# Optimization experiments

Measured on AMD Instinct MI355X. Metric: run time of the kernel, lower is better.

## Reference

```python
import jax, jax.numpy as jnp
import numpy as np

B = 8          # batch
RES = 64       # resolution (H = W)
DIM = 512      # channels
HEADS = 8
HD = DIM // HEADS   # 64
HSP, WSP = RES, 8   # idx=0: H_sp=resolution, W_sp=split_size
NH, NW = RES // HSP, RES // WSP   # windows per axis


def setup_inputs() -> dict:
    key = jax.random.key(0)
    k1, k2, k3 = jax.random.split(key, 3)
    qkv = jax.random.normal(k1, (3, B, RES * RES, DIM), dtype=jnp.float32)
    lepe_w = jax.random.normal(k2, (DIM, 1, 3, 3), dtype=jnp.float32) * 0.1
    lepe_b = jax.random.normal(k3, (DIM,), dtype=jnp.float32) * 0.1
    return {"qkv": qkv, "lepe_w": lepe_w, "lepe_b": lepe_b}


def _to_windows(t):
    # [B, L, C] row-major -> [B*NH*NW, HSP*WSP, C]; equivalent to the
    # block-diagonal flex_attention mask grouping (y//H_sp, x//W_sp).
    t = t.reshape(B, NH, HSP, NW, WSP, DIM)
    return t.transpose(0, 1, 3, 2, 4, 5).reshape(B * NH * NW, HSP * WSP, DIM)


def _from_windows(t):
    t = t.reshape(B, NH, NW, HSP, WSP, DIM).transpose(0, 1, 3, 2, 4, 5)
    return t.reshape(B, RES * RES, DIM)


def reference(qkv, lepe_w, lepe_b):
    q, k, v = qkv[0], qkv[1], qkv[2]            # each [B, L, C]
    qw, kw, vw = _to_windows(q), _to_windows(k), _to_windows(v)

    # LePE: depthwise 3x3 conv on v laid out per-window as [n, C, HSP, WSP]
    vimg = vw.transpose(0, 2, 1).reshape(-1, DIM, HSP, WSP)
    lepe = jax.lax.conv_general_dilated(
        vimg, lepe_w, window_strides=(1, 1), padding='SAME',
        dimension_numbers=('NCHW', 'OIHW', 'NCHW'), feature_group_count=DIM)
    lepe = lepe + lepe_b[None, :, None, None]
    lepe = lepe.reshape(-1, DIM, HSP * WSP).transpose(0, 2, 1)  # [n, T, C]

    def split_heads(t):
        return t.reshape(t.shape[0], t.shape[1], HEADS, HD)

    qh, kh, vh, lh = map(split_heads, (qw, kw, vw, lepe))
    scale = 1.0 / np.sqrt(HD).astype(np.float32)  # flex_attention default scale
    scores = jnp.einsum('wqhd,wkhd->whqk', qh, kh) * scale
    attn = jax.nn.softmax(scores, axis=-1)
    out = jnp.einsum('whqk,wkhd->wqhd', attn, vh) + lh   # [n, T, H, hd]
    out = out.reshape(out.shape[0], out.shape[1], DIM)
    return _from_windows(out)
```

## Files before the change

kernel.cpp:

```cpp
#include <hip/hip_runtime.h>
#include <hip/hip_bf16.h>

#define DIMV 512
#define HDV  64
#define VSTR 524
#define VT_BASE 65536
#define SMEM_B (VT_BASE + 64 * VSTR * 2)

typedef __bf16 bf16x8_t __attribute__((ext_vector_type(8)));
typedef float f32x4_t __attribute__((ext_vector_type(4)));

union Frag { bf16x8_t v; unsigned short u[8]; unsigned int w[4]; uint2 d[2]; uint4 q; };

static __device__ __forceinline__ unsigned short f2bf(float f) {
  return __builtin_bit_cast(unsigned short, (__bf16)f);
}
static __device__ __forceinline__ float bf2f(unsigned int h) {
  return __builtin_bit_cast(float, h << 16);
}
static __device__ __forceinline__ uint2 pack4(const float4 f) {
  uint2 r;
  r.x = (unsigned)f2bf(f.x) | ((unsigned)f2bf(f.y) << 16);
  r.y = (unsigned)f2bf(f.z) | ((unsigned)f2bf(f.w) << 16);
  return r;
}

#define BARRIER_NODRAIN() asm volatile("s_waitcnt lgkmcnt(0)\n\ts_barrier" ::: "memory")

__global__ __launch_bounds__(1024, 4)
void lepe_attn_kernel(const float* __restrict__ qkv,
                      const float* __restrict__ lw,
                      const float* __restrict__ lb,
                      float* __restrict__ out)
{
  __shared__ __align__(16) unsigned char smem[SMEM_B];

  const int wb   = blockIdx.x;
  const int win  = wb >> 2;
  const int bat  = win >> 3;
  const int nw   = win & 7;
  const int headbase = (wb & 3) << 1;

  const int tid  = threadIdx.x;
  const int wave = tid >> 6, lane = tid & 63;
  const int l15  = lane & 15, g = lane >> 4;

  const float* qptr = qkv;
  const float* kptr = qkv + 16777216;
  const float* vptr = qkv + 33554432;
  const int rowbase = bat * 4096;

  auto grow = [&](int tok) -> int {
    return rowbase + ((tok >> 3) << 6) + (nw << 3) + (tok & 7);
  };

  const int s_t = tid >> 4;
  const int s_c = (tid & 15) * 4;
  const size_t TSTRIDE = 262144;
  const size_t base_st = (size_t)grow(s_t) * DIMV + s_c;

  const int lr    = s_t & 31;
  const int tb0   = (s_t >> 5) * 4096;
  const int kfrag = (lr >> 4) * 2048 + (s_c >> 5) * 1024
                  + ((lr & 15) + 16 * ((s_c >> 3) & 3)) * 16 + (s_c & 7) * 2;

  unsigned short* vt = (unsigned short*)(smem + VT_BASE);

  float4 ck0, ck1, cv0, cv1;
  float4 qin[8];

  auto issueC = [&](int head, int c) {
    const float* kgp = kptr + base_st + head * HDV;
    const float* vgp = vptr + base_st + head * HDV;
    ck0 = *(const float4*)(kgp + (size_t)(2 * c) * TSTRIDE);
    ck1 = *(const float4*)(kgp + (size_t)(2 * c + 1) * TSTRIDE);
    cv0 = *(const float4*)(vgp + (size_t)(2 * c) * TSTRIDE);
    cv1 = *(const float4*)(vgp + (size_t)(2 * c + 1) * TSTRIDE);
  };
  auto writeC = [&](int c) {
    *(uint2*)(smem + c * 16384 + tb0 + kfrag)        = pack4(ck0);
    *(uint2*)(smem + c * 16384 + 8192 + tb0 + kfrag) = pack4(ck1);
    int t0 = s_t + 128 * c;
    vt[(s_c + 0) * VSTR + t0] = f2bf(cv0.x);
    vt[(s_c + 1) * VSTR + t0] = f2bf(cv0.y);
    vt[(s_c + 2) * VSTR + t0] = f2bf(cv0.z);
    vt[(s_c + 3) * VSTR + t0] = f2bf(cv0.w);
    int t1 = t0 + 64;
    vt[(s_c + 0) * VSTR + t1] = f2bf(cv1.x);
    vt[(s_c + 1) * VSTR + t1] = f2bf(cv1.y);
    vt[(s_c + 2) * VSTR + t1] = f2bf(cv1.z);
    vt[(s_c + 3) * VSTR + t1] = f2bf(cv1.w);
  };

  const float QSC = 0.1803368801f;
  const int qbase = wave * 32;
  size_t qoff[2];
  qoff[0] = (size_t)grow(qbase + l15) * DIMV;
  qoff[1] = (size_t)grow(qbase + 16 + l15) * DIMV;

  Frag qf[2][2];
  auto issueQ = [&](int head) {
    #pragma unroll
    for (int qi = 0; qi < 2; ++qi) {
      const float* qp = qptr + qoff[qi] + head * HDV;
      #pragma unroll
      for (int kc = 0; kc < 2; ++kc) {
        qin[qi * 4 + kc * 2 + 0] = *(const float4*)(qp + kc * 32 + 8 * g);
        qin[qi * 4 + kc * 2 + 1] = *(const float4*)(qp + kc * 32 + 8 * g + 4);
      }
    }
  };
  auto buildQF = [&]() {
    #pragma unroll
    for (int qi = 0; qi < 2; ++qi)
      #pragma unroll
      for (int kc = 0; kc < 2; ++kc) {
        const float4 f0 = qin[qi * 4 + kc * 2 + 0];
        const float4 f1 = qin[qi * 4 + kc * 2 + 1];
        qf[qi][kc].u[0] = f2bf(f0.x * QSC); qf[qi][kc].u[1] = f2bf(f0.y * QSC);
        qf[qi][kc].u[2] = f2bf(f0.z * QSC); qf[qi][kc].u[3] = f2bf(f0.w * QSC);
        qf[qi][kc].u[4] = f2bf(f1.x * QSC); qf[qi][kc].u[5] = f2bf(f1.y * QSC);
        qf[qi][kc].u[6] = f2bf(f1.z * QSC); qf[qi][kc].u[7] = f2bf(f1.w * QSC);
      }
  };

  issueC(headbase, 0);
  issueQ(headbase);
  writeC(0);
  buildQF();
  __syncthreads();

  const f32x4_t zero4 = {0.f, 0.f, 0.f, 0.f};
  const unsigned char* kfb = smem + lane * 16;

  #pragma unroll
  for (int p = 0; p < 2; ++p) {
    const int head = headbase + p;

    f32x4_t ot[4][2];
    #pragma unroll
    for (int di = 0; di < 4; ++di)
      #pragma unroll
      for (int qi = 0; qi < 2; ++qi) ot[di][qi] = zero4;
    float lsum[2] = {0.f, 0.f};

    #pragma unroll
    for (int c = 0; c < 4; ++c) {
      if (c < 3) issueC(head, c + 1);

      #pragma unroll
      for (int t4 = 0; t4 < 4; ++t4) {
        const int kt = c * 4 + t4;

        Frag kf[2][2];
        #pragma unroll
        for (int ki = 0; ki < 2; ++ki)
          #pragma unroll
          for (int kc = 0; kc < 2; ++kc)
            kf[ki][kc].q = *(const uint4*)(kfb + kt * 4096 + ki * 2048 + kc * 1024);

        f32x4_t st[2][2];
        #pragma unroll
        for (int ki = 0; ki < 2; ++ki)
          #pragma unroll
          for (int qi = 0; qi < 2; ++qi) st[ki][qi] = zero4;

        __builtin_amdgcn_s_setprio(1);
        #pragma unroll
        for (int kc = 0; kc < 2; ++kc)
          #pragma unroll
          for (int ki = 0; ki < 2; ++ki)
            #pragma unroll
            for (int qi = 0; qi < 2; ++qi)
              st[ki][qi] = __builtin_amdgcn_mfma_f32_16x16x32_bf16(
                  kf[ki][kc].v, qf[qi][kc].v, st[ki][qi], 0, 0, 0);
        __builtin_amdgcn_s_setprio(0);

        #pragma unroll
        for (int ki = 0; ki < 2; ++ki)
          #pragma unroll
          for (int qi = 0; qi < 2; ++qi) {
            f32x4_t s = st[ki][qi];
            #pragma unroll
            for (int r = 0; r < 4; ++r) {
              float pr = __builtin_amdgcn_exp2f(s[r]);
              s[r] = pr;
              lsum[qi] += pr;
            }
            st[ki][qi] = s;
          }

        Frag vf[4];
        #pragma unroll
        for (int di = 0; di < 4; ++di) {
          const unsigned char* vp = smem + VT_BASE + (di * 16 + l15) * (VSTR * 2)
                                    + kt * 64 + 8 * g;
          vf[di].d[0] = *(const uint2*)(vp);
          vf[di].d[1] = *(const uint2*)(vp + 32);
        }

        __builtin_amdgcn_s_setprio(1);
        #pragma unroll
        for (int qi = 0; qi < 2; ++qi) {
          Frag pb;
          #pragma unroll
          for (int r = 0; r < 4; ++r) {
            pb.u[r]     = f2bf(st[0][qi][r]);
            pb.u[4 + r] = f2bf(st[1][qi][r]);
          }
          #pragma unroll
          for (int di = 0; di < 4; ++di)
            ot[di][qi] = __builtin_amdgcn_mfma_f32_16x16x32_bf16(
                vf[di].v, pb.v, ot[di][qi], 0, 0, 0);
        }
        __builtin_amdgcn_s_setprio(0);
      }

      if (c < 3) { writeC(c + 1); BARRIER_NODRAIN(); }
    }

    float rl[2];
    #pragma unroll
    for (int qi = 0; qi < 2; ++qi) {
      float s = lsum[qi];
      s += __shfl_xor(s, 16, 64);
      s += __shfl_xor(s, 32, 64);
      rl[qi] = 1.0f / s;
    }

    float lout[32];
    {
      float wgt[9];
      const float* wp = lw + (size_t)(head * HDV + lane) * 9;
      #pragma unroll
      for (int i = 0; i < 9; ++i) wgt[i] = wp[i];
      const float bias = lb[head * HDV + lane];
      const int yb = wave * 4;

      float rm[8], rc[8], rp2[8];
      auto loadrow = [&](int y, float* dst) {
        if ((unsigned)y < 64u) {
          const unsigned char* pp = smem + VT_BASE + lane * (VSTR * 2) + y * 16;
          unsigned a0 = *(const unsigned*)(pp);
          unsigned a1 = *(const unsigned*)(pp + 4);
          unsigned a2 = *(const unsigned*)(pp + 8);
          unsigned a3 = *(const unsigned*)(pp + 12);
          dst[0] = bf2f(a0 & 0xffffu); dst[1] = bf2f(a0 >> 16);
          dst[2] = bf2f(a1 & 0xffffu); dst[3] = bf2f(a1 >> 16);
          dst[4] = bf2f(a2 & 0xffffu); dst[5] = bf2f(a2 >> 16);
          dst[6] = bf2f(a3 & 0xffffu); dst[7] = bf2f(a3 >> 16);
        } else {
          #pragma unroll
          for (int x = 0; x < 8; ++x) dst[x] = 0.f;
        }
      };
      loadrow(yb - 1, rm);
      loadrow(yb, rc);
      #pragma unroll
      for (int yy = 0; yy < 4; ++yy) {
        loadrow(yb + yy + 1, rp2);
        #pragma unroll
        for (int x = 0; x < 8; ++x) {
          float acc = bias;
          if (x > 0) acc += rm[x-1]*wgt[0] + rc[x-1]*wgt[3] + rp2[x-1]*wgt[6];
          acc += rm[x]*wgt[1] + rc[x]*wgt[4] + rp2[x]*wgt[7];
          if (x < 7) acc += rm[x+1]*wgt[2] + rc[x+1]*wgt[5] + rp2[x+1]*wgt[8];
          lout[yy * 8 + x] = acc;
        }
        #pragma unroll
        for (int x = 0; x < 8; ++x) { rm[x] = rc[x]; rc[x] = rp2[x]; }
      }
    }

    BARRIER_NODRAIN();

    unsigned char* bp = smem + wave * 4352;
    #pragma unroll
    for (int t = 0; t < 32; ++t)
      *(unsigned short*)(bp + t * 136 + 2 * lane) = f2bf(lout[t]);

    if (p == 0) issueC(headbase + 1, 0);

    #pragma unroll
    for (int qi = 0; qi < 2; ++qi) {
      const float rlq = rl[qi];
      const int tl = qi * 16 + l15;
      float* op = out + (size_t)grow(qbase + tl) * DIMV + head * HDV;
      #pragma unroll
      for (int di = 0; di < 4; ++di) {
        uint2 lv = *(const uint2*)(bp + tl * 136 + di * 32 + 8 * g);
        float4 o;
        o.x = ot[di][qi][0] * rlq + bf2f(lv.x & 0xffffu);
        o.y = ot[di][qi][1] * rlq + bf2f(lv.x >> 16);
        o.z = ot[di][qi][2] * rlq + bf2f(lv.y & 0xffffu);
        o.w = ot[di][qi][3] * rlq + bf2f(lv.y >> 16);
        *(float4*)(op + di * 16 + 4 * g) = o;
      }
    }

    if (p == 0) {
      BARRIER_NODRAIN();
      writeC(0);
      issueQ(headbase + 1);
      buildQF();
      BARRIER_NODRAIN();
    }
  }
}

extern "C" void kernel_launch(void* const* d_in, const int* in_sizes, int n_in,
                              void* d_out, int out_size, void* d_ws, size_t ws_size,
                              hipStream_t stream) {
  const float* qkv = (const float*)d_in[0];
  const float* lw  = (const float*)d_in[1];
  const float* lb  = (const float*)d_in[2];
  float* out = (float*)d_out;
  (void)in_sizes; (void)n_in; (void)out_size; (void)d_ws; (void)ws_size;

  dim3 grid(256);
  dim3 block(1024);
  hipLaunchKernelGGL(lepe_attn_kernel, grid, block, 0, stream, qkv, lw, lb, out);
}
```

Baseline: 85.71 us.

## Split work to one head per block with swizzled V layout and K ring

Each block now handles a single head instead of two, doubling the grid to 512 blocks for better CU occupancy on the large GPU. K is streamed through a two-slot double-buffered ring, while all of V is loaded up front into an XOR-swizzled transposed layout that replaces the padded stride. LDS use drops from about 130KB to 80KB. The cost is that per-block setup and LePE weight loads are no longer amortized across two heads, and the serialized head loop is gone.

```diff
diff --git a/kernel.cpp b/kernel.cpp
--- a/kernel.cpp
+++ b/kernel.cpp
@@ -3,9 +3,9 @@
 
 #define DIMV 512
 #define HDV  64
-#define VSTR 524
-#define VT_BASE 65536
-#define SMEM_B (VT_BASE + 64 * VSTR * 2)
+#define KRING_B 16384
+#define VT_BASE KRING_B
+#define SMEM_B (VT_BASE + 65536)
 
 typedef __bf16 bf16x8_t __attribute__((ext_vector_type(8)));
 typedef float f32x4_t __attribute__((ext_vector_type(4)));
@@ -35,11 +35,10 @@
 {
   __shared__ __align__(16) unsigned char smem[SMEM_B];
 
-  const int wb   = blockIdx.x;
-  const int win  = wb >> 2;
+  const int head = blockIdx.x & 7;
+  const int win  = blockIdx.x >> 3;
   const int bat  = win >> 3;
   const int nw   = win & 7;
-  const int headbase = (wb & 3) << 1;
 
   const int tid  = threadIdx.x;
   const int wave = tid >> 6, lane = tid & 63;
@@ -56,254 +55,226 @@
 
   const int s_t = tid >> 4;
   const int s_c = (tid & 15) * 4;
-  const size_t TSTRIDE = 262144;
-  const size_t base_st = (size_t)grow(s_t) * DIMV + s_c;
-
-  const int lr    = s_t & 31;
-  const int tb0   = (s_t >> 5) * 4096;
-  const int kfrag = (lr >> 4) * 2048 + (s_c >> 5) * 1024
-                  + ((lr & 15) + 16 * ((s_c >> 3) & 3)) * 16 + (s_c & 7) * 2;
-
-  unsigned short* vt = (unsigned short*)(smem + VT_BASE);
-
-  float4 ck0, ck1, cv0, cv1;
-  float4 qin[8];
-
-  auto issueC = [&](int head, int c) {
-    const float* kgp = kptr + base_st + head * HDV;
-    const float* vgp = vptr + base_st + head * HDV;
-    ck0 = *(const float4*)(kgp + (size_t)(2 * c) * TSTRIDE);
-    ck1 = *(const float4*)(kgp + (size_t)(2 * c + 1) * TSTRIDE);
-    cv0 = *(const float4*)(vgp + (size_t)(2 * c) * TSTRIDE);
-    cv1 = *(const float4*)(vgp + (size_t)(2 * c + 1) * TSTRIDE);
+  const size_t GSTRIDE = 262144;
+  const float* kg = kptr + (size_t)grow(s_t) * DIMV + head * HDV + s_c;
+  const float* vg = vptr + (size_t)grow(s_t) * DIMV + head * HDV + s_c;
+
+  const int lr  = s_t & 31;
+  const int kwb = (s_t >> 5) * 4096 + (lr >> 4) * 2048 + (s_c >> 5) * 1024
+                + ((lr & 15) + 16 * ((s_c >> 3) & 3)) * 16 + (s_c & 7) * 2;
+
+  float4 kc4;
+  auto issueK = [&](int c) { kc4 = *(const float4*)(kg + (size_t)c * GSTRIDE); };
+  auto writeK = [&](int c) {
+    *(uint2*)(smem + (c & 1) * 8192 + kwb) = pack4(kc4);
   };
-  auto writeC = [&](int c) {
-    *(uint2*)(smem + c * 16384 + tb0 + kfrag)        = pack4(ck0);
-    *(uint2*)(smem + c * 16384 + 8192 + tb0 + kfrag) = pack4(ck1);
-    int t0 = s_t + 128 * c;
-    vt[(s_c + 0) * VSTR + t0] = f2bf(cv0.x);
-    vt[(s_c + 1) * VSTR + t0] = f2bf(cv0.y);
-    vt[(s_c + 2) * VSTR + t0] = f2bf(cv0.z);
-    vt[(s_c + 3) * VSTR + t0] = f2bf(cv0.w);
-    int t1 = t0 + 64;
-    vt[(s_c + 0) * VSTR + t1] = f2bf(cv1.x);
-    vt[(s_c + 1) * VSTR + t1] = f2bf(cv1.y);
-    vt[(s_c + 2) * VSTR + t1] = f2bf(cv1.z);
-    vt[(s_c + 3) * VSTR + t1] = f2bf(cv1.w);
-  };
+
+  issueK(0);
+  float4 vin[8];
+  #pragma unroll
+  for (int j = 0; j < 8; ++j) vin[j] = *(const float4*)(vg + (size_t)j * GSTRIDE);
 
   const float QSC = 0.1803368801f;
   const int qbase = wave * 32;
-  size_t qoff[2];
-  qoff[0] = (size_t)grow(qbase + l15) * DIMV;
-  qoff[1] = (size_t)grow(qbase + 16 + l15) * DIMV;
+  float4 qin[8];
+  #pragma unroll
+  for (int qi = 0; qi < 2; ++qi) {
+    const float* qp = qptr + (size_t)grow(qbase + qi * 16 + l15) * DIMV + head * HDV;
+    #pragma unroll
+    for (int kc = 0; kc < 2; ++kc) {
+      qin[qi * 4 + kc * 2 + 0] = *(const float4*)(qp + kc * 32 + 8 * g);
+      qin[qi * 4 + kc * 2 + 1] = *(const float4*)(qp + kc * 32 + 8 * g + 4);
+    }
+  }
+
+  writeK(0);
+  #pragma unroll
+  for (int j = 0; j < 8; ++j) {
+    const int t2 = 2 * (j * 64 + s_t);
+    float fv[4] = {vin[j].x, vin[j].y, vin[j].z, vin[j].w};
+    #pragma unroll
+    for (int i = 0; i < 4; ++i) {
+      const int d = s_c + i;
+      *(unsigned short*)(smem + VT_BASE + d * 1024 + (t2 ^ ((d & 7) << 4))) = f2bf(fv[i]);
+    }
+  }
 
   Frag qf[2][2];
-  auto issueQ = [&](int head) {
-    #pragma unroll
-    for (int qi = 0; qi < 2; ++qi) {
-      const float* qp = qptr + qoff[qi] + head * HDV;
-      #pragma unroll
-      for (int kc = 0; kc < 2; ++kc) {
-        qin[qi * 4 + kc * 2 + 0] = *(const float4*)(qp + kc * 32 + 8 * g);
-        qin[qi * 4 + kc * 2 + 1] = *(const float4*)(qp + kc * 32 + 8 * g + 4);
-      }
-    }
-  };
-  auto buildQF = [&]() {
-    #pragma unroll
-    for (int qi = 0; qi < 2; ++qi)
-      #pragma unroll
-      for (int kc = 0; kc < 2; ++kc) {
-        const float4 f0 = qin[qi * 4 + kc * 2 + 0];
-        const float4 f1 = qin[qi * 4 + kc * 2 + 1];
-        qf[qi][kc].u[0] = f2bf(f0.x * QSC); qf[qi][kc].u[1] = f2bf(f0.y * QSC);
-        qf[qi][kc].u[2] = f2bf(f0.z * QSC); qf[qi][kc].u[3] = f2bf(f0.w * QSC);
-        qf[qi][kc].u[4] = f2bf(f1.x * QSC); qf[qi][kc].u[5] = f2bf(f1.y * QSC);
-        qf[qi][kc].u[6] = f2bf(f1.z * QSC); qf[qi][kc].u[7] = f2bf(f1.w * QSC);
-      }
-  };
-
-  issueC(headbase, 0);
-  issueQ(headbase);
-  writeC(0);
-  buildQF();
+  #pragma unroll
+  for (int qi = 0; qi < 2; ++qi)
+    #pragma unroll
+    for (int kc = 0; kc < 2; ++kc) {
+      const float4 f0 = qin[qi * 4 + kc * 2 + 0];
+      const float4 f1 = qin[qi * 4 + kc * 2 + 1];
+      qf[qi][kc].u[0] = f2bf(f0.x * QSC); qf[qi][kc].u[1] = f2bf(f0.y * QSC);
+      qf[qi][kc].u[2] = f2bf(f0.z * QSC); qf[qi][kc].u[3] = f2bf(f0.w * QSC);
+      qf[qi][kc].u[4] = f2bf(f1.x * QSC); qf[qi][kc].u[5] = f2bf(f1.y * QSC);
+      qf[qi][kc].u[6] = f2bf(f1.z * QSC); qf[qi][kc].u[7] = f2bf(f1.w * QSC);
+    }
+
   __syncthreads();
 
   const f32x4_t zero4 = {0.f, 0.f, 0.f, 0.f};
-  const unsigned char* kfb = smem + lane * 16;
-
-  #pragma unroll
-  for (int p = 0; p < 2; ++p) {
-    const int head = headbase + p;
-
-    f32x4_t ot[4][2];
-    #pragma unroll
-    for (int di = 0; di < 4; ++di)
-      #pragma unroll
-      for (int qi = 0; qi < 2; ++qi) ot[di][qi] = zero4;
-    float lsum[2] = {0.f, 0.f};
-
-    #pragma unroll
-    for (int c = 0; c < 4; ++c) {
-      if (c < 3) issueC(head, c + 1);
-
-      #pragma unroll
-      for (int t4 = 0; t4 < 4; ++t4) {
-        const int kt = c * 4 + t4;
-
-        Frag kf[2][2];
+  f32x4_t ot[4][2];
+  #pragma unroll
+  for (int di = 0; di < 4; ++di)
+    #pragma unroll
+    for (int qi = 0; qi < 2; ++qi) ot[di][qi] = zero4;
+  float lsum[2] = {0.f, 0.f};
+
+  const int vswz = (l15 & 7) << 4;
+
+  for (int c = 0; c < 8; ++c) {
+    if (c < 7) issueK(c + 1);
+
+    #pragma unroll
+    for (int t2i = 0; t2i < 2; ++t2i) {
+      const int kt = c * 2 + t2i;
+      const unsigned char* kbase = smem + (c & 1) * 8192 + t2i * 4096 + lane * 16;
+
+      Frag kf[2][2];
+      #pragma unroll
+      for (int ki = 0; ki < 2; ++ki)
+        #pragma unroll
+        for (int kc = 0; kc < 2; ++kc)
+          kf[ki][kc].q = *(const uint4*)(kbase + ki * 2048 + kc * 1024);
+
+      f32x4_t st[2][2];
+      #pragma unroll
+      for (int ki = 0; ki < 2; ++ki)
+        #pragma unroll
+        for (int qi = 0; qi < 2; ++qi) st[ki][qi] = zero4;
+
+      __builtin_amdgcn_s_setprio(1);
+      #pragma unroll
+      for (int kc = 0; kc < 2; ++kc)
         #pragma unroll
         for (int ki = 0; ki < 2; ++ki)
           #pragma unroll
-          for (int kc = 0; kc < 2; ++kc)
-            kf[ki][kc].q = *(const uint4*)(kfb + kt * 4096 + ki * 2048 + kc * 1024);
-
-        f32x4_t st[2][2];
-        #pragma unroll
-        for (int ki = 0; ki < 2; ++ki)
-          #pragma unroll
-          for (int qi = 0; qi < 2; ++qi) st[ki][qi] = zero4;
-
-        __builtin_amdgcn_s_setprio(1);
-        #pragma unroll
-        for (int kc = 0; kc < 2; ++kc)
-          #pragma unroll
-          for (int ki = 0; ki < 2; ++ki)
-            #pragma unroll
-            for (int qi = 0; qi < 2; ++qi)
-              st[ki][qi] = __builtin_amdgcn_mfma_f32_16x16x32_bf16(
-                  kf[ki][kc].v, qf[qi][kc].v, st[ki][qi], 0, 0, 0);
-        __builtin_amdgcn_s_setprio(0);
-
-        #pragma unroll
-        for (int ki = 0; ki < 2; ++ki)
-          #pragma unroll
-          for (int qi = 0; qi < 2; ++qi) {
-            f32x4_t s = st[ki][qi];
-            #pragma unroll
-            for (int r = 0; r < 4; ++r) {
-              float pr = __builtin_amdgcn_exp2f(s[r]);
-              s[r] = pr;
-              lsum[qi] += pr;
-            }
-            st[ki][qi] = s;
-          }
-
-        Frag vf[4];
-        #pragma unroll
-        for (int di = 0; di < 4; ++di) {
-          const unsigned char* vp = smem + VT_BASE + (di * 16 + l15) * (VSTR * 2)
-                                    + kt * 64 + 8 * g;
-          vf[di].d[0] = *(const uint2*)(vp);
-          vf[di].d[1] = *(const uint2*)(vp + 32);
-        }
-
-        __builtin_amdgcn_s_setprio(1);
+          for (int qi = 0; qi < 2; ++qi)
+            st[ki][qi] = __builtin_amdgcn_mfma_f32_16x16x32_bf16(
+                kf[ki][kc].v, qf[qi][kc].v, st[ki][qi], 0, 0, 0);
+      __builtin_amdgcn_s_setprio(0);
+
+      #pragma unroll
+      for (int ki = 0; ki < 2; ++ki)
         #pragma unroll
         for (int qi = 0; qi < 2; ++qi) {
-          Frag pb;
+          f32x4_t s = st[ki][qi];
           #pragma unroll
           for (int r = 0; r < 4; ++r) {
-            pb.u[r]     = f2bf(st[0][qi][r]);
-            pb.u[4 + r] = f2bf(st[1][qi][r]);
+            float pr = __builtin_amdgcn_exp2f(s[r]);
+            s[r] = pr;
+            lsum[qi] += pr;
           }
-          #pragma unroll
-          for (int di = 0; di < 4; ++di)
-            ot[di][qi] = __builtin_amdgcn_mfma_f32_16x16x32_bf16(
-                vf[di].v, pb.v, ot[di][qi], 0, 0, 0);
+          st[ki][qi] = s;
         }
-        __builtin_amdgcn_s_setprio(0);
-      }
-
-      if (c < 3) { writeC(c + 1); BARRIER_NODRAIN(); }
-    }
-
-    float rl[2];
-    #pragma unroll
-    for (int qi = 0; qi < 2; ++qi) {
-      float s = lsum[qi];
-      s += __shfl_xor(s, 16, 64);
-      s += __shfl_xor(s, 32, 64);
-      rl[qi] = 1.0f / s;
-    }
-
-    float lout[32];
-    {
-      float wgt[9];
-      const float* wp = lw + (size_t)(head * HDV + lane) * 9;
-      #pragma unroll
-      for (int i = 0; i < 9; ++i) wgt[i] = wp[i];
-      const float bias = lb[head * HDV + lane];
-      const int yb = wave * 4;
-
-      float rm[8], rc[8], rp2[8];
-      auto loadrow = [&](int y, float* dst) {
-        if ((unsigned)y < 64u) {
-          const unsigned char* pp = smem + VT_BASE + lane * (VSTR * 2) + y * 16;
-          unsigned a0 = *(const unsigned*)(pp);
-          unsigned a1 = *(const unsigned*)(pp + 4);
-          unsigned a2 = *(const unsigned*)(pp + 8);
-          unsigned a3 = *(const unsigned*)(pp + 12);
-          dst[0] = bf2f(a0 & 0xffffu); dst[1] = bf2f(a0 >> 16);
-          dst[2] = bf2f(a1 & 0xffffu); dst[3] = bf2f(a1 >> 16);
-          dst[4] = bf2f(a2 & 0xffffu); dst[5] = bf2f(a2 >> 16);
-          dst[6] = bf2f(a3 & 0xffffu); dst[7] = bf2f(a3 >> 16);
-        } else {
-          #pragma unroll
-          for (int x = 0; x < 8; ++x) dst[x] = 0.f;
+
+      Frag vf[4];
+      #pragma unroll
+      for (int di = 0; di < 4; ++di) {
+        const unsigned char* vrow = smem + VT_BASE + (di * 16 + l15) * 1024;
+        vf[di].d[0] = *(const uint2*)(vrow + ((kt * 64 + 8 * g) ^ vswz));
+        vf[di].d[1] = *(const uint2*)(vrow + ((kt * 64 + 32 + 8 * g) ^ vswz));
+      }
+
+      __builtin_amdgcn_s_setprio(1);
+      #pragma unroll
+      for (int qi = 0; qi < 2; ++qi) {
+        Frag pb;
+        #pragma unroll
+        for (int r = 0; r < 4; ++r) {
+          pb.u[r]     = f2bf(st[0][qi][r]);
+          pb.u[4 + r] = f2bf(st[1][qi][r]);
         }
-      };
-      loadrow(yb - 1, rm);
-      loadrow(yb, rc);
-      #pragma unroll
-      for (int yy = 0; yy < 4; ++yy) {
-        loadrow(yb + yy + 1, rp2);
-        #pragma unroll
-        for (int x = 0; x < 8; ++x) {
-          float acc = bias;
-          if (x > 0) acc += rm[x-1]*wgt[0] + rc[x-1]*wgt[3] + rp2[x-1]*wgt[6];
-          acc += rm[x]*wgt[1] + rc[x]*wgt[4] + rp2[x]*wgt[7];
-          if (x < 7) acc += rm[x+1]*wgt[2] + rc[x+1]*wgt[5] + rp2[x+1]*wgt[8];
-          lout[yy * 8 + x] = acc;
-        }
-        #pragma unroll
-        for (int x = 0; x < 8; ++x) { rm[x] = rc[x]; rc[x] = rp2[x]; }
-      }
-    }
-
-    BARRIER_NODRAIN();
-
-    unsigned char* bp = smem + wave * 4352;
-    #pragma unroll
-    for (int t = 0; t < 32; ++t)
-      *(unsigned short*)(bp + t * 136 + 2 * lane) = f2bf(lout[t]);
-
-    if (p == 0) issueC(headbase + 1, 0);
-
-    #pragma unroll
-    for (int qi = 0; qi < 2; ++qi) {
-      const float rlq = rl[qi];
-      const int tl = qi * 16 + l15;
-      float* op = out + (size_t)grow(qbase + tl) * DIMV + head * HDV;
-      #pragma unroll
-      for (int di = 0; di < 4; ++di) {
-        uint2 lv = *(const uint2*)(bp + tl * 136 + di * 32 + 8 * g);
-        float4 o;
-        o.x = ot[di][qi][0] * rlq + bf2f(lv.x & 0xffffu);
-        o.y = ot[di][qi][1] * rlq + bf2f(lv.x >> 16);
-        o.z = ot[di][qi][2] * rlq + bf2f(lv.y & 0xffffu);
-        o.w = ot[di][qi][3] * rlq + bf2f(lv.y >> 16);
-        *(float4*)(op + di * 16 + 4 * g) = o;
-      }
-    }
-
-    if (p == 0) {
-      BARRIER_NODRAIN();
-      writeC(0);
-      issueQ(headbase + 1);
-      buildQF();
-      BARRIER_NODRAIN();
+        #pragma unroll
+        for (int di = 0; di < 4; ++di)
+          ot[di][qi] = __builtin_amdgcn_mfma_f32_16x16x32_bf16(
+              vf[di].v, pb.v, ot[di][qi], 0, 0, 0);
+      }
+      __builtin_amdgcn_s_setprio(0);
+    }
+
+    if (c < 7) { writeK(c + 1); BARRIER_NODRAIN(); }
+  }
+
+  float rl[2];
+  #pragma unroll
+  for (int qi = 0; qi < 2; ++qi) {
+    float s = lsum[qi];
+    s += __shfl_xor(s, 16, 64);
+    s += __shfl_xor(s, 32, 64);
+    rl[qi] = 1.0f / s;
+  }
+
+  float lout[32];
+  {
+    float wgt[9];
+    const float* wp = lw + (size_t)(head * HDV + lane) * 9;
+    #pragma unroll
+    for (int i = 0; i < 9; ++i) wgt[i] = wp[i];
+    const float bias = lb[head * HDV + lane];
+    const int yb = wave * 4;
+    const unsigned char* vrow = smem + VT_BASE + lane * 1024;
+    const int lsw = (lane & 7) << 4;
+
+    float rm[8], rc[8], rp2[8];
+    auto loadrow = [&](int y, float* dst) {
+      if ((unsigned)y < 64u) {
+        uint4 a = *(const uint4*)(vrow + ((y * 16) ^ lsw));
+        dst[0] = bf2f(a.x & 0xffffu); dst[1] = bf2f(a.x >> 16);
+        dst[2] = bf2f(a.y & 0xffffu); dst[3] = bf2f(a.y >> 16);
+        dst[4] = bf2f(a.z & 0xffffu); dst[5] = bf2f(a.z >> 16);
+        dst[6] = bf2f(a.w & 0xffffu); dst[7] = bf2f(a.w >> 16);
+      } else {
+        #pragma unroll
+        for (int x = 0; x < 8; ++x) dst[x] = 0.f;
+      }
+    };
+    loadrow(yb - 1, rm);
+    loadrow(yb, rc);
+    #pragma unroll
+    for (int yy = 0; yy < 4; ++yy) {
+      loadrow(yb + yy + 1, rp2);
+      #pragma unroll
+      for (int x = 0; x < 8; ++x) {
+        float acc = bias;
+        if (x > 0) acc += rm[x-1]*wgt[0] + rc[x-1]*wgt[3] + rp2[x-1]*wgt[6];
+        acc += rm[x]*wgt[1] + rc[x]*wgt[4] + rp2[x]*wgt[7];
+        if (x < 7) acc += rm[x+1]*wgt[2] + rc[x+1]*wgt[5] + rp2[x+1]*wgt[8];
+        lout[yy * 8 + x] = acc;
+      }
+      #pragma unroll
+      for (int x = 0; x < 8; ++x) { rm[x] = rc[x]; rc[x] = rp2[x]; }
+    }
+  }
+
+  BARRIER_NODRAIN();
+
+  #pragma unroll
+  for (int t = 0; t < 32; ++t) {
+    const int tok = qbase + t;
+    *(unsigned short*)(smem + VT_BASE + tok * 128 + ((2 * lane) ^ ((tok & 7) << 4)))
+        = f2bf(lout[t]);
+  }
+  BARRIER_NODRAIN();
+
+  #pragma unroll
+  for (int qi = 0; qi < 2; ++qi) {
+    const float rlq = rl[qi];
+    const int tok = qbase + qi * 16 + l15;
+    const unsigned char* brow = smem + VT_BASE + tok * 128;
+    const int bsw = (l15 & 7) << 4;
+    float* op = out + (size_t)grow(tok) * DIMV + head * HDV;
+    #pragma unroll
+    for (int di = 0; di < 4; ++di) {
+      uint2 lv = *(const uint2*)(brow + ((di * 32 + 8 * g) ^ bsw));
+      float4 o;
+      o.x = ot[di][qi][0] * rlq + bf2f(lv.x & 0xffffu);
+      o.y = ot[di][qi][1] * rlq + bf2f(lv.x >> 16);
+      o.z = ot[di][qi][2] * rlq + bf2f(lv.y & 0xffffu);
+      o.w = ot[di][qi][3] * rlq + bf2f(lv.y >> 16);
+      *(float4*)(op + di * 16 + 4 * g) = o;
     }
   }
 }
@@ -317,7 +288,7 @@
   float* out = (float*)d_out;
   (void)in_sizes; (void)n_in; (void)out_size; (void)d_ws; (void)ws_size;
 
-  dim3 grid(256);
+  dim3 grid(512);
   dim3 block(1024);
   hipLaunchKernelGGL(lepe_attn_kernel, grid, block, 0, stream, qkv, lw, lb, out);
 }
```

New measurement: 83.93 us. -2.1%, faster.
